# Performance work log

Measured on AMD Instinct MI355X. Metric: run time of the kernel, lower is better.

The kernel has to match this reference:

```python
import jax, jax.numpy as jnp
import numpy as np

B, T, D, H = 2, 2048, 1024, 16

def setup_inputs() -> dict:
    key = jax.random.key(0)
    k0, k1, k2, k3 = jax.random.split(key, 4)
    s = 0.02
    return {
        "x": jax.random.normal(k0, (B, T, D), dtype=jnp.float32),
        "Wqkv": jax.random.normal(k1, (3 * D, D), dtype=jnp.float32) * s,
        "Wout": jax.random.normal(k2, (D, D), dtype=jnp.float32) * s,
        "bout": jax.random.normal(k3, (D,), dtype=jnp.float32) * s,
    }

def reference(x, Wqkv, Wout, bout):
    b, t, d = x.shape
    h = H
    dh = d // h
    qkv = x @ Wqkv.T  # [b,t,3d]
    q, k, v = jnp.split(qkv, 3, axis=-1)
    def merge_heads(z):
        return z.reshape(b, t, h, dh).transpose(0, 2, 1, 3)  # [b,h,t,dh]
    q, k, v = map(merge_heads, (q, k, v))
    scale = dh ** -0.5
    dots = jnp.einsum('bhid,bhjd->bhij', q, k) * scale  # [b,h,t,t]
    causal_mask = jnp.triu(jnp.ones((t, t), dtype=bool), 1)
    dots = jnp.where(causal_mask, -jnp.inf, dots)
    attn = jax.nn.softmax(dots, axis=-1)
    out = jnp.einsum('bhij,bhjd->bhid', attn, v)  # [b,h,t,dh]
    out = out.transpose(0, 2, 1, 3).reshape(b, t, d)
    return out @ Wout.T + bout
```

## Files before the change

kernel.cpp:

```cpp
#include <hip/hip_runtime.h>
#include <hip/hip_bf16.h>
#include <math.h>

typedef __bf16 bf16x8 __attribute__((ext_vector_type(8)));
typedef float f32x4 __attribute__((ext_vector_type(4)));
typedef unsigned short u16;
typedef unsigned int u32;

#define EXP2F(x) __builtin_amdgcn_exp2f(x)

constexpr int Bz = 2, T = 2048, D = 1024, H = 16;
constexpr int M = Bz * T;
constexpr int NQKV = 3 * D;
constexpr float SCALE2 = 0.125f * 1.44269504089f;

#define GLD_LDS16(g, l) __builtin_amdgcn_global_load_lds( \
    (__attribute__((address_space(1))) void*)(g),          \
    (__attribute__((address_space(3))) void*)(l), 16, 0, 0)

__global__ void cvt_all_kernel(const float* __restrict__ x,
                               const float* __restrict__ wq,
                               const float* __restrict__ wo,
                               u16* __restrict__ xb, u16* __restrict__ wqb,
                               u16* __restrict__ wob) {
  constexpr int NX = M * D / 4;
  constexpr int NQ = NQKV * D / 4;
  constexpr int NW = D * D / 4;
  constexpr int TOT = NX + NQ + NW;
  int i = blockIdx.x * blockDim.x + threadIdx.x;
  int stride = gridDim.x * blockDim.x;
  for (; i < TOT; i += stride) {
    const float4* src;
    u16* dst;
    int j;
    if (i < NX) { src = (const float4*)x; dst = xb; j = i; }
    else if (i < NX + NQ) { src = (const float4*)wq; dst = wqb; j = i - NX; }
    else { src = (const float4*)wo; dst = wob; j = i - NX - NQ; }
    float4 f = src[j];
    ushort4 u;
    u.x = __builtin_bit_cast(u16, (__bf16)f.x);
    u.y = __builtin_bit_cast(u16, (__bf16)f.y);
    u.z = __builtin_bit_cast(u16, (__bf16)f.z);
    u.w = __builtin_bit_cast(u16, (__bf16)f.w);
    ((ushort4*)dst)[j] = u;
  }
}

template <bool FP32OUT, bool QSCALE>
__global__ __launch_bounds__(256, 2)
void gemm_bt(const u16* __restrict__ A, const u16* __restrict__ Bm,
             u16* __restrict__ outb, float* __restrict__ outf,
             const float* __restrict__ bias, int K, int ldc) {
  __shared__ __align__(16) u16 sA[128 * 64];
  __shared__ __align__(16) u16 sB[128 * 64];
  const int tid = threadIdx.x;
  const int lane = tid & 63;
  const int wid = tid >> 6;
  const int wr = wid >> 1, wc = wid & 1;

  const int nwg = gridDim.x * gridDim.y;
  const int flat = blockIdx.y * gridDim.x + blockIdx.x;
  const int cpx = nwg >> 3;
  const int swz = (flat & 7) * cpx + (flat >> 3);
  const int bx = swz % gridDim.x;
  const int by = swz / gridDim.x;

  const int row0 = by * 128;
  const int col0 = bx * 128;

  f32x4 acc[4][4];
#pragma unroll
  for (int m = 0; m < 4; ++m)
#pragma unroll
    for (int n = 0; n < 4; ++n) acc[m][n] = (f32x4){0.f, 0.f, 0.f, 0.f};

  const int nk = K >> 6;
  for (int kt = 0; kt < nk; ++kt) {
    const int k0 = kt << 6;
#pragma unroll
    for (int i = 0; i < 4; ++i) {
      int off = i * 4096 + tid * 16;
      int r = off >> 7;
      int cs = (off >> 4) & 7;
      int c = cs ^ (r & 7);
      const u16* ga = A + (size_t)(row0 + r) * K + k0 + c * 8;
      const u16* gb = Bm + (size_t)(col0 + r) * K + k0 + c * 8;
      u16* la = sA + (i * 4096 + (tid & ~63) * 16) / 2;
      u16* lb = sB + (i * 4096 + (tid & ~63) * 16) / 2;
      GLD_LDS16(ga, la);
      GLD_LDS16(gb, lb);
    }
    __syncthreads();
#pragma unroll
    for (int kk = 0; kk < 2; ++kk) {
      bf16x8 af[4], bfv[4];
#pragma unroll
      for (int m = 0; m < 4; ++m) {
        int r = wr * 64 + m * 16 + (lane & 15);
        int cs = (kk * 4 + (lane >> 4)) ^ (r & 7);
        af[m] = *(const bf16x8*)(sA + r * 64 + cs * 8);
      }
#pragma unroll
      for (int n = 0; n < 4; ++n) {
        int r = wc * 64 + n * 16 + (lane & 15);
        int cs = (kk * 4 + (lane >> 4)) ^ (r & 7);
        bfv[n] = *(const bf16x8*)(sB + r * 64 + cs * 8);
      }
#pragma unroll
      for (int m = 0; m < 4; ++m)
#pragma unroll
        for (int n = 0; n < 4; ++n)
          acc[m][n] = __builtin_amdgcn_mfma_f32_16x16x32_bf16(
              af[m], bfv[n], acc[m][n], 0, 0, 0);
    }
    __syncthreads();
  }

  const int orow0 = row0 + wr * 64;
  const int ocol0 = col0 + wc * 64;
#pragma unroll
  for (int m = 0; m < 4; ++m)
#pragma unroll
    for (int n = 0; n < 4; ++n)
#pragma unroll
      for (int j = 0; j < 4; ++j) {
        int rr = orow0 + m * 16 + (lane >> 4) * 4 + j;
        int cc = ocol0 + n * 16 + (lane & 15);
        if (FP32OUT) {
          outf[(size_t)rr * ldc + cc] = acc[m][n][j] + bias[cc];
        } else {
          float v = acc[m][n][j];
          if (QSCALE && cc < D) v *= SCALE2;
          outb[(size_t)rr * ldc + cc] = __builtin_bit_cast(u16, (__bf16)v);
        }
      }
}

__global__ __launch_bounds__(256, 3)
void flash_kernel(const u16* __restrict__ qkv, u16* __restrict__ attn_out) {
  __shared__ __align__(16) u16 sK[2][64 * 64];
  __shared__ __align__(16) u16 sVt[2][64 * 72];
  __shared__ __align__(16) u16 sP[4][16][72];

  const int tid = threadIdx.x;
  const int lane = tid & 63;
  const int l15 = lane & 15;
  const int hi = lane >> 4;
  const int w = tid >> 6;
  const int bh = blockIdx.x;
  const int b = bh >> 4, h = bh & 15;
  const int qt = (gridDim.y - 1) - blockIdx.y;
  const int q0 = qt * 64;
  const int nv = qt + 1;

  const size_t base = (size_t)b * T * 3072;
  const u16* qp = qkv + base + 0 * 1024 + h * 64;
  const u16* kp = qkv + base + 1 * 1024 + h * 64;
  const u16* vp = qkv + base + 2 * 1024 + h * 64;

  ushort4 vr[2][2];
  auto stageK = [&](u16* dst, int kt) {
#pragma unroll
    for (int i = 0; i < 2; ++i) {
      int off = i * 4096 + tid * 16;
      int r = off >> 7;
      int cs = (off >> 4) & 7;
      int c = cs ^ (r & 7);
      GLD_LDS16(kp + (size_t)(kt * 64 + r) * 3072 + c * 8,
                dst + (i * 4096 + (tid & ~63) * 16) / 2);
    }
  };
  auto loadV = [&](int kt) {
#pragma unroll
    for (int i = 0; i < 2; ++i) {
      const u16* gsrc = vp + (size_t)(kt * 64 + lane) * 3072 + (i * 4 + w) * 8;
      vr[i][0] = ((const ushort4*)gsrc)[0];
      vr[i][1] = ((const ushort4*)gsrc)[1];
    }
  };
  auto writeV = [&](u16* dst) {
#pragma unroll
    for (int i = 0; i < 2; ++i) {
      int c = i * 4 + w;
      dst[(c * 8 + 0) * 72 + lane] = vr[i][0].x;
      dst[(c * 8 + 1) * 72 + lane] = vr[i][0].y;
      dst[(c * 8 + 2) * 72 + lane] = vr[i][0].z;
      dst[(c * 8 + 3) * 72 + lane] = vr[i][0].w;
      dst[(c * 8 + 4) * 72 + lane] = vr[i][1].x;
      dst[(c * 8 + 5) * 72 + lane] = vr[i][1].y;
      dst[(c * 8 + 6) * 72 + lane] = vr[i][1].z;
      dst[(c * 8 + 7) * 72 + lane] = vr[i][1].w;
    }
  };

  bf16x8 qf[2];
#pragma unroll
  for (int kk = 0; kk < 2; ++kk)
    qf[kk] = *(const bf16x8*)(qp + (size_t)(q0 + w * 16 + l15) * 3072 +
                              kk * 32 + hi * 8);

  f32x4 o_acc[4];
#pragma unroll
  for (int n = 0; n < 4; ++n) o_acc[n] = (f32x4){0.f, 0.f, 0.f, 0.f};
  float l_run = 0.f;

  stageK(sK[0], 0);
  loadV(0);
  writeV(sVt[0]);
  __syncthreads();

  for (int v = 0; v < nv; ++v) {
    const int cur = v & 1;
    const int k0 = v * 64;
    if (v + 1 < nv) {
      stageK(sK[cur ^ 1], v + 1);
      loadV(v + 1);
    }

    bf16x8 kf[2][4];
#pragma unroll
    for (int kk = 0; kk < 2; ++kk)
#pragma unroll
      for (int n = 0; n < 4; ++n) {
        int rk = n * 16 + l15;
        int cs = (kk * 4 + hi) ^ (rk & 7);
        kf[kk][n] = *(const bf16x8*)(&sK[cur][rk * 64 + cs * 8]);
      }
    bf16x8 vf[2][4];
#pragma unroll
    for (int ks = 0; ks < 2; ++ks)
#pragma unroll
      for (int n = 0; n < 4; ++n)
        vf[ks][n] = *(const bf16x8*)(
            &sVt[cur][(n * 16 + l15) * 72 + ks * 32 + hi * 8]);

    f32x4 sc[4];
#pragma unroll
    for (int n = 0; n < 4; ++n) sc[n] = (f32x4){0.f, 0.f, 0.f, 0.f};
    __builtin_amdgcn_s_setprio(1);
#pragma unroll
    for (int kk = 0; kk < 2; ++kk)
#pragma unroll
      for (int n = 0; n < 4; ++n)
        sc[n] = __builtin_amdgcn_mfma_f32_16x16x32_bf16(kf[kk][n], qf[kk],
                                                        sc[n], 0, 0, 0);
    __builtin_amdgcn_s_setprio(0);

    const bool diag = (v == nv - 1);
    const int qrow = q0 + w * 16 + l15;
    if (diag) {
#pragma unroll
      for (int n = 0; n < 4; ++n)
#pragma unroll
        for (int r = 0; r < 4; ++r) {
          int kpos = k0 + n * 16 + hi * 4 + r;
          if (kpos > qrow) sc[n][r] = -INFINITY;
        }
    }

    float sum = 0.f;
#pragma unroll
    for (int n = 0; n < 4; ++n) {
      float p0 = EXP2F(sc[n][0]);
      float p1 = EXP2F(sc[n][1]);
      float p2 = EXP2F(sc[n][2]);
      float p3 = EXP2F(sc[n][3]);
      sum += (p0 + p1) + (p2 + p3);
      u32 w01 = ((u32)__builtin_bit_cast(u16, (__bf16)p1) << 16) |
                __builtin_bit_cast(u16, (__bf16)p0);
      u32 w23 = ((u32)__builtin_bit_cast(u16, (__bf16)p3) << 16) |
                __builtin_bit_cast(u16, (__bf16)p2);
      *(u32*)(&sP[w][l15][n * 16 + hi * 4 + 0]) = w01;
      *(u32*)(&sP[w][l15][n * 16 + hi * 4 + 2]) = w23;
    }
    l_run += sum;

    __builtin_amdgcn_s_setprio(1);
#pragma unroll
    for (int ks = 0; ks < 2; ++ks) {
      bf16x8 pf = *(const bf16x8*)(&sP[w][l15][ks * 32 + hi * 8]);
#pragma unroll
      for (int n = 0; n < 4; ++n)
        o_acc[n] = __builtin_amdgcn_mfma_f32_16x16x32_bf16(pf, vf[ks][n],
                                                           o_acc[n], 0, 0, 0);
    }
    __builtin_amdgcn_s_setprio(0);

    if (v + 1 < nv) writeV(sVt[cur ^ 1]);
    if (v + 1 < nv) __syncthreads();
  }

  l_run += __shfl_xor(l_run, 16, 64);
  l_run += __shfl_xor(l_run, 32, 64);

#pragma unroll
  for (int j = 0; j < 4; ++j) {
    float lj = __shfl(l_run, hi * 4 + j, 64);
    float inv = 1.f / lj;
    int row = q0 + w * 16 + hi * 4 + j;
#pragma unroll
    for (int n = 0; n < 4; ++n) {
      int cc = h * 64 + n * 16 + l15;
      attn_out[((size_t)b * T + row) * 1024 + cc] =
          __builtin_bit_cast(u16, (__bf16)(o_acc[n][j] * inv));
    }
  }
}

extern "C" void kernel_launch(void* const* d_in, const int* in_sizes, int n_in,
                              void* d_out, int out_size, void* d_ws,
                              size_t ws_size, hipStream_t stream) {
  (void)in_sizes; (void)n_in; (void)out_size; (void)ws_size;
  const float* x = (const float*)d_in[0];
  const float* Wqkv = (const float*)d_in[1];
  const float* Wout = (const float*)d_in[2];
  const float* bout = (const float*)d_in[3];
  float* out = (float*)d_out;

  char* ws = (char*)d_ws;
  u16* x_bf = (u16*)(ws + 0);
  u16* wqkv_bf = (u16*)(ws + 8388608);
  u16* wout_bf = (u16*)(ws + 14680064);
  u16* qkvb = (u16*)(ws + 16777216);
  u16* aout = (u16*)(ws + 41943040);

  cvt_all_kernel<<<2048, 256, 0, stream>>>(x, Wqkv, Wout, x_bf, wqkv_bf,
                                           wout_bf);

  gemm_bt<false, true><<<dim3(NQKV / 128, M / 128), 256, 0, stream>>>(
      x_bf, wqkv_bf, qkvb, nullptr, nullptr, D, NQKV);

  flash_kernel<<<dim3(Bz * H, T / 64), 256, 0, stream>>>(qkvb, aout);

  gemm_bt<true, false><<<dim3(D / 128, M / 128), 256, 0, stream>>>(
      aout, wout_bf, nullptr, out, bout, D, D);
}
```

Baseline: 101.0 us.

## Load K fragments directly from global memory instead of staging in LDS

Drops the shared-memory K double buffer and its async global-to-LDS staging. Each wave now reads its K MFMA fragments straight from global memory every iteration. This frees LDS and the occupancy hint rises from 3 to 5 blocks per SM. It also packs the two 32-bit P stores into one 64-bit store and tree-reduces the row sums. The risk is that the four waves each reload the same K tile from global memory or cache, and those loads are no longer prefetched a tile ahead, which can expose latency.

Result: slower. 209.9 us (+107.8%).

```diff
diff --git a/kernel.cpp b/kernel.cpp
--- a/kernel.cpp
+++ b/kernel.cpp
@@ -6,6 +6,7 @@
 typedef float f32x4 __attribute__((ext_vector_type(4)));
 typedef unsigned short u16;
 typedef unsigned int u32;
+typedef u32 u32x2 __attribute__((ext_vector_type(2)));
 
 #define EXP2F(x) __builtin_amdgcn_exp2f(x)
 
@@ -136,9 +137,8 @@
       }
 }
 
-__global__ __launch_bounds__(256, 3)
+__global__ __launch_bounds__(256, 5)
 void flash_kernel(const u16* __restrict__ qkv, u16* __restrict__ attn_out) {
-  __shared__ __align__(16) u16 sK[2][64 * 64];
   __shared__ __align__(16) u16 sVt[2][64 * 72];
   __shared__ __align__(16) u16 sP[4][16][72];
 
@@ -159,17 +159,6 @@
   const u16* vp = qkv + base + 2 * 1024 + h * 64;
 
   ushort4 vr[2][2];
-  auto stageK = [&](u16* dst, int kt) {
-#pragma unroll
-    for (int i = 0; i < 2; ++i) {
-      int off = i * 4096 + tid * 16;
-      int r = off >> 7;
-      int cs = (off >> 4) & 7;
-      int c = cs ^ (r & 7);
-      GLD_LDS16(kp + (size_t)(kt * 64 + r) * 3072 + c * 8,
-                dst + (i * 4096 + (tid & ~63) * 16) / 2);
-    }
-  };
   auto loadV = [&](int kt) {
 #pragma unroll
     for (int i = 0; i < 2; ++i) {
@@ -204,28 +193,25 @@
   for (int n = 0; n < 4; ++n) o_acc[n] = (f32x4){0.f, 0.f, 0.f, 0.f};
   float l_run = 0.f;
 
-  stageK(sK[0], 0);
   loadV(0);
   writeV(sVt[0]);
   __syncthreads();
 
+  const u16* kfbase = kp + (size_t)l15 * 3072 + hi * 8;
+
   for (int v = 0; v < nv; ++v) {
     const int cur = v & 1;
     const int k0 = v * 64;
-    if (v + 1 < nv) {
-      stageK(sK[cur ^ 1], v + 1);
-      loadV(v + 1);
-    }
+    if (v + 1 < nv) loadV(v + 1);
 
     bf16x8 kf[2][4];
 #pragma unroll
     for (int kk = 0; kk < 2; ++kk)
 #pragma unroll
-      for (int n = 0; n < 4; ++n) {
-        int rk = n * 16 + l15;
-        int cs = (kk * 4 + hi) ^ (rk & 7);
-        kf[kk][n] = *(const bf16x8*)(&sK[cur][rk * 64 + cs * 8]);
-      }
+      for (int n = 0; n < 4; ++n)
+        kf[kk][n] = *(const bf16x8*)(kfbase +
+            (size_t)(k0 + n * 16) * 3072 + kk * 32);
+
     bf16x8 vf[2][4];
 #pragma unroll
     for (int ks = 0; ks < 2; ++ks)
@@ -258,22 +244,22 @@
         }
     }
 
-    float sum = 0.f;
+    float psum[4];
 #pragma unroll
     for (int n = 0; n < 4; ++n) {
       float p0 = EXP2F(sc[n][0]);
       float p1 = EXP2F(sc[n][1]);
       float p2 = EXP2F(sc[n][2]);
       float p3 = EXP2F(sc[n][3]);
-      sum += (p0 + p1) + (p2 + p3);
-      u32 w01 = ((u32)__builtin_bit_cast(u16, (__bf16)p1) << 16) |
-                __builtin_bit_cast(u16, (__bf16)p0);
-      u32 w23 = ((u32)__builtin_bit_cast(u16, (__bf16)p3) << 16) |
-                __builtin_bit_cast(u16, (__bf16)p2);
-      *(u32*)(&sP[w][l15][n * 16 + hi * 4 + 0]) = w01;
-      *(u32*)(&sP[w][l15][n * 16 + hi * 4 + 2]) = w23;
-    }
-    l_run += sum;
+      psum[n] = (p0 + p1) + (p2 + p3);
+      u32x2 pw;
+      pw.x = ((u32)__builtin_bit_cast(u16, (__bf16)p1) << 16) |
+             __builtin_bit_cast(u16, (__bf16)p0);
+      pw.y = ((u32)__builtin_bit_cast(u16, (__bf16)p3) << 16) |
+             __builtin_bit_cast(u16, (__bf16)p2);
+      *(u32x2*)(&sP[w][l15][n * 16 + hi * 4]) = pw;
+    }
+    l_run += (psum[0] + psum[1]) + (psum[2] + psum[3]);
 
     __builtin_amdgcn_s_setprio(1);
 #pragma unroll
@@ -286,8 +272,10 @@
     }
     __builtin_amdgcn_s_setprio(0);
 
-    if (v + 1 < nv) writeV(sVt[cur ^ 1]);
-    if (v + 1 < nv) __syncthreads();
+    if (v + 1 < nv) {
+      writeV(sVt[cur ^ 1]);
+      __syncthreads();
+    }
   }
 
   l_run += __shfl_xor(l_run, 16, 64);
```

## Split long causal query tiles across two blocks and combine partial outputs

Applied to the files above, without the earlier changes.

Query tiles 16-31, the ones with the longest causal key ranges, are now split into two halves of the key range, each handled by a separate block. Each half writes unnormalized bf16 partial outputs and row sums into reused workspace, and a new combine kernel adds and normalizes them. Because the softmax uses no running max, the halves can be summed directly. The aim is to even out per-block work and shorten the critical path of the flash kernel, at the cost of an extra launch, extra global traffic for the partials, and bf16 rounding of the partials.

Result: slower. 109.0 us (+7.9%).

```diff
diff --git a/kernel.cpp b/kernel.cpp
--- a/kernel.cpp
+++ b/kernel.cpp
@@ -6,6 +6,7 @@
 typedef float f32x4 __attribute__((ext_vector_type(4)));
 typedef unsigned short u16;
 typedef unsigned int u32;
+typedef u16 u16x8 __attribute__((ext_vector_type(8)));
 
 #define EXP2F(x) __builtin_amdgcn_exp2f(x)
 
@@ -137,7 +138,8 @@
 }
 
 __global__ __launch_bounds__(256, 3)
-void flash_kernel(const u16* __restrict__ qkv, u16* __restrict__ attn_out) {
+void flash_kernel(const u16* __restrict__ qkv, u16* __restrict__ attn_out,
+                  u16* __restrict__ opart, float* __restrict__ lpart) {
   __shared__ __align__(16) u16 sK[2][64 * 64];
   __shared__ __align__(16) u16 sVt[2][64 * 72];
   __shared__ __align__(16) u16 sP[4][16][72];
@@ -149,9 +151,22 @@
   const int w = tid >> 6;
   const int bh = blockIdx.x;
   const int b = bh >> 4, h = bh & 15;
-  const int qt = (gridDim.y - 1) - blockIdx.y;
+
+  const int y = blockIdx.y;
+  int qt, v0, v1, half;
+  if (y < 32) {
+    qt = 31 - (y & 15);
+    const int m = (qt + 1) >> 1;
+    half = y >> 4;
+    v0 = half ? m : 0;
+    v1 = half ? qt + 1 : m;
+  } else {
+    qt = 47 - y;
+    half = -1;
+    v0 = 0;
+    v1 = qt + 1;
+  }
   const int q0 = qt * 64;
-  const int nv = qt + 1;
 
   const size_t base = (size_t)b * T * 3072;
   const u16* qp = qkv + base + 0 * 1024 + h * 64;
@@ -204,15 +219,15 @@
   for (int n = 0; n < 4; ++n) o_acc[n] = (f32x4){0.f, 0.f, 0.f, 0.f};
   float l_run = 0.f;
 
-  stageK(sK[0], 0);
-  loadV(0);
+  stageK(sK[0], v0);
+  loadV(v0);
   writeV(sVt[0]);
   __syncthreads();
 
-  for (int v = 0; v < nv; ++v) {
-    const int cur = v & 1;
+  for (int v = v0; v < v1; ++v) {
+    const int cur = (v - v0) & 1;
     const int k0 = v * 64;
-    if (v + 1 < nv) {
+    if (v + 1 < v1) {
       stageK(sK[cur ^ 1], v + 1);
       loadV(v + 1);
     }
@@ -246,7 +261,7 @@
                                                         sc[n], 0, 0, 0);
     __builtin_amdgcn_s_setprio(0);
 
-    const bool diag = (v == nv - 1);
+    const bool diag = (v == qt);
     const int qrow = q0 + w * 16 + l15;
     if (diag) {
 #pragma unroll
@@ -286,25 +301,73 @@
     }
     __builtin_amdgcn_s_setprio(0);
 
-    if (v + 1 < nv) writeV(sVt[cur ^ 1]);
-    if (v + 1 < nv) __syncthreads();
+    if (v + 1 < v1) writeV(sVt[cur ^ 1]);
+    if (v + 1 < v1) __syncthreads();
   }
 
   l_run += __shfl_xor(l_run, 16, 64);
   l_run += __shfl_xor(l_run, 32, 64);
 
-#pragma unroll
-  for (int j = 0; j < 4; ++j) {
-    float lj = __shfl(l_run, hi * 4 + j, 64);
-    float inv = 1.f / lj;
-    int row = q0 + w * 16 + hi * 4 + j;
-#pragma unroll
-    for (int n = 0; n < 4; ++n) {
-      int cc = h * 64 + n * 16 + l15;
-      attn_out[((size_t)b * T + row) * 1024 + cc] =
-          __builtin_bit_cast(u16, (__bf16)(o_acc[n][j] * inv));
-    }
-  }
+  if (half >= 0) {
+    const int p = (qt - 16) * 32 + bh;
+    const int slot = p * 2 + half;
+    if (hi == 0) lpart[slot * 64 + w * 16 + l15] = l_run;
+    u16* Op = opart + (size_t)slot * 64 * 64;
+#pragma unroll
+    for (int j = 0; j < 4; ++j) {
+      int row = w * 16 + hi * 4 + j;
+#pragma unroll
+      for (int n = 0; n < 4; ++n)
+        Op[row * 64 + n * 16 + l15] =
+            __builtin_bit_cast(u16, (__bf16)o_acc[n][j]);
+    }
+  } else {
+#pragma unroll
+    for (int j = 0; j < 4; ++j) {
+      float lj = __shfl(l_run, hi * 4 + j, 64);
+      float inv = 1.f / lj;
+      int row = q0 + w * 16 + hi * 4 + j;
+#pragma unroll
+      for (int n = 0; n < 4; ++n) {
+        int cc = h * 64 + n * 16 + l15;
+        attn_out[((size_t)b * T + row) * 1024 + cc] =
+            __builtin_bit_cast(u16, (__bf16)(o_acc[n][j] * inv));
+      }
+    }
+  }
+}
+
+__global__ __launch_bounds__(256)
+void combine_kernel(const u16* __restrict__ opart,
+                    const float* __restrict__ lpart,
+                    u16* __restrict__ attn_out) {
+  const int p = blockIdx.x;
+  const int t = threadIdx.x;
+  const int qt = 16 + (p >> 5);
+  const int bh = p & 31;
+  const int b = bh >> 4, h = bh & 15;
+  const int row = t >> 2;
+  const int c0 = (t & 3) * 16;
+
+  const u16* O0 = opart + ((size_t)(p * 2 + 0) * 64 + row) * 64 + c0;
+  const u16* O1 = opart + ((size_t)(p * 2 + 1) * 64 + row) * 64 + c0;
+  const float inv = 1.f /
+      (lpart[(p * 2 + 0) * 64 + row] + lpart[(p * 2 + 1) * 64 + row]);
+
+  u16x8 out[2];
+#pragma unroll
+  for (int g = 0; g < 2; ++g) {
+    bf16x8 a = *(const bf16x8*)(O0 + g * 8);
+    bf16x8 c = *(const bf16x8*)(O1 + g * 8);
+#pragma unroll
+    for (int i = 0; i < 8; ++i) {
+      float v = ((float)a[i] + (float)c[i]) * inv;
+      out[g][i] = __builtin_bit_cast(u16, (__bf16)v);
+    }
+  }
+  u16* dst = attn_out + ((size_t)b * T + qt * 64 + row) * 1024 + h * 64 + c0;
+  *(u16x8*)(dst + 0) = out[0];
+  *(u16x8*)(dst + 8) = out[1];
 }
 
 extern "C" void kernel_launch(void* const* d_in, const int* in_sizes, int n_in,
@@ -323,6 +386,8 @@
   u16* wout_bf = (u16*)(ws + 14680064);
   u16* qkvb = (u16*)(ws + 16777216);
   u16* aout = (u16*)(ws + 41943040);
+  u16* opart = x_bf;
+  float* lpart = (float*)wqkv_bf;
 
   cvt_all_kernel<<<2048, 256, 0, stream>>>(x, Wqkv, Wout, x_bf, wqkv_bf,
                                            wout_bf);
@@ -330,7 +395,9 @@
   gemm_bt<false, true><<<dim3(NQKV / 128, M / 128), 256, 0, stream>>>(
       x_bf, wqkv_bf, qkvb, nullptr, nullptr, D, NQKV);
 
-  flash_kernel<<<dim3(Bz * H, T / 64), 256, 0, stream>>>(qkvb, aout);
+  flash_kernel<<<dim3(Bz * H, 48), 256, 0, stream>>>(qkvb, aout, opart,
+                                                     lpart);
+  combine_kernel<<<512, 256, 0, stream>>>(opart, lpart, aout);
 
   gemm_bt<true, false><<<dim3(D / 128, M / 128), 256, 0, stream>>>(
       aout, wout_bf, nullptr, out, bout, D, D);
```
